# Optimization experiments

Measured on AMD Instinct MI355X. Metric: run time of the kernel, lower is better.

The kernel has to match this reference:

```python
import jax, jax.numpy as jnp
import numpy as np

B, N, E = 4, 20000, 320000
DA, DB, H, OUT = 64, 64, 128, 1  # feature dims, hidden_dim, output_dim; DA+DB == H


def setup_inputs() -> dict:
    key = jax.random.key(0)
    ks = jax.random.split(key, 9)
    feat_a = jax.random.normal(ks[0], (B, N, DA), dtype=jnp.float32)
    feat_b = jax.random.normal(ks[1], (B, N, DB), dtype=jnp.float32)
    edge_index = jax.random.randint(ks[2], (2, E), 0, N)
    s = 1.0 / np.sqrt(H)
    W_gcn = jax.random.normal(ks[3], (H, H), dtype=jnp.float32) * s
    b_gcn = jnp.zeros((H,), dtype=jnp.float32)
    W1 = jax.random.normal(ks[4], (H, H), dtype=jnp.float32) * s
    b1 = jax.random.normal(ks[5], (H,), dtype=jnp.float32) * 0.01
    W2 = jax.random.normal(ks[6], (H, OUT), dtype=jnp.float32) * s
    b2 = jnp.zeros((OUT,), dtype=jnp.float32)
    return {"feat_a": feat_a, "feat_b": feat_b, "edge_index": edge_index,
            "W_gcn": W_gcn, "b_gcn": b_gcn, "W1": W1, "b1": b1, "W2": W2, "b2": b2}


def _gcn_conv(x, src, dst, W, b):
    # x: [B, N, H_in]; GCNConv: out = D^-1/2 (A+I) D^-1/2 (x W) + b
    n = x.shape[1]
    loops = jnp.arange(n)
    src_sl = jnp.concatenate([src, loops])  # add self-loops
    dst_sl = jnp.concatenate([dst, loops])
    deg = jax.ops.segment_sum(jnp.ones_like(src_sl, dtype=x.dtype), dst_sl, num_segments=n)
    dinv = jnp.where(deg > 0, jax.lax.rsqrt(deg), 0.0)
    norm = dinv[src_sl] * dinv[dst_sl]  # [E+N]
    h = x @ W  # [B, N, H]

    def agg(hb):  # hb: [N, H]
        msgs = hb[src_sl] * norm[:, None]  # gather + scale, [E+N, H]
        return jax.ops.segment_sum(msgs, dst_sl, num_segments=n)  # scatter-add

    return jax.vmap(agg)(h) + b


def reference(feat_a, feat_b, edge_index, W_gcn, b_gcn, W1, b1, W2, b2):
    combined = jnp.concatenate([feat_a, feat_b], axis=-1)  # [B, N, H]
    gcn_out = _gcn_conv(combined, edge_index[0], edge_index[1], W_gcn, b_gcn)
    pooled = gcn_out.mean(axis=1)  # mean over nodes -> [B, H]
    hid = jax.nn.relu(pooled @ W1 + b1)  # dropout is identity in eval
    logits = hid @ W2 + b2  # [B, 1]
    return logits
```

## Files before the change

### kernel.cpp

```cpp
#include <hip/hip_runtime.h>

#define NB 4
#define NN 20000
#define NE 320000
#define HH 128

#define EBLK 64
#define HTHR 1024
#define CHUNKS 128
#define WTHR 512
#define PER ((NN + CHUNKS - 1) / CHUNKS)
#define TOTW (CHUNKS * NB)

#define OFF_PDEG 0
#define OFF_DINV (EBLK * NN)
#define OFF_PS   (OFF_DINV + NN)
#define OFF_V    (OFF_PS + EBLK * NN)
#define OFF_CNT  (OFF_V + NB * HH)

__global__ void __launch_bounds__(HTHR) deg_hist_kernel(
        const int* __restrict__ dst, float* __restrict__ pdeg) {
    __shared__ float hist[NN];
    const int t = threadIdx.x, bk = blockIdx.x;
    for (int i = t; i < NN; i += HTHR) hist[i] = 0.0f;
    __syncthreads();
    for (int e = bk * HTHR + t; e < NE; e += EBLK * HTHR)
        atomicAdd(&hist[dst[e]], 1.0f);
    __syncthreads();
    float* out = pdeg + (size_t)bk * NN;
    for (int i = t; i < NN; i += HTHR) out[i] = hist[i];
}

__global__ void reduce_deg_kernel(const float* __restrict__ pdeg,
                                  float* __restrict__ dinv,
                                  float* __restrict__ v, int* __restrict__ counter) {
    if (blockIdx.x == 0) {
        v[threadIdx.x] = 0.0f;
        v[threadIdx.x + 256] = 0.0f;
        if (threadIdx.x == 0) *counter = 0;
    }
    const int n = blockIdx.x * 256 + threadIdx.x;
    if (n >= NN) return;
    float acc = 1.0f;
    #pragma unroll 8
    for (int c = 0; c < EBLK; ++c) acc += pdeg[(size_t)c * NN + n];
    dinv[n] = rsqrtf(acc);
}

__global__ void __launch_bounds__(HTHR) s_hist_kernel(
        const int* __restrict__ src, const int* __restrict__ dst,
        const float* __restrict__ dinv, float* __restrict__ ps) {
    __shared__ float hist[NN];
    const int t = threadIdx.x, bk = blockIdx.x;
    for (int i = t; i < NN; i += HTHR) hist[i] = 0.0f;
    __syncthreads();
    for (int e = bk * HTHR + t; e < NE; e += EBLK * HTHR)
        atomicAdd(&hist[src[e]], dinv[dst[e]]);
    __syncthreads();
    float* out = ps + (size_t)bk * NN;
    for (int i = t; i < NN; i += HTHR) out[i] = hist[i];
}

__global__ void __launch_bounds__(WTHR) wsum_mlp_kernel(
        const float* __restrict__ fa, const float* __restrict__ fb,
        const float* __restrict__ dinv, const float* __restrict__ ps,
        const float* __restrict__ Wg, const float* __restrict__ bg,
        const float* __restrict__ W1, const float* __restrict__ b1,
        const float* __restrict__ W2, const float* __restrict__ b2,
        float* __restrict__ v, int* __restrict__ counter,
        float* __restrict__ out) {
    __shared__ float wl[PER];
    __shared__ float4 smem[WTHR];
    __shared__ int lastflag;
    const int t = threadIdx.x;
    const int c = blockIdx.x, b = blockIdx.y;
    const int n0 = c * PER;
    const int n1 = min(NN, n0 + PER);
    const int cnt = n1 - n0;

    for (int i = t; i < cnt; i += WTHR) {
        const int n = n0 + i;
        float acc = 0.0f;
        #pragma unroll 8
        for (int cc = 0; cc < EBLK; ++cc) acc += ps[(size_t)cc * NN + n];
        const float di = dinv[n];
        wl[i] = di * (di + acc);
    }
    __syncthreads();

    const int g = t >> 5;
    const int q = t & 31;
    const float* base = (q < 16)
        ? (fa + (size_t)b * NN * 64 + (size_t)q * 4)
        : (fb + (size_t)b * NN * 64 + (size_t)(q - 16) * 4);

    float4 acc = make_float4(0.f, 0.f, 0.f, 0.f);
    for (int n = n0 + g; n < n1; n += 16) {
        float wn = wl[n - n0];
        float4 x = *reinterpret_cast<const float4*>(base + (size_t)n * 64);
        acc.x += wn * x.x; acc.y += wn * x.y; acc.z += wn * x.z; acc.w += wn * x.w;
    }

    smem[t] = acc;
    __syncthreads();
    if (t < 32) {
        float4 r = smem[t];
        #pragma unroll
        for (int gg = 1; gg < 16; ++gg) {
            float4 o = smem[gg * 32 + t];
            r.x += o.x; r.y += o.y; r.z += o.z; r.w += o.w;
        }
        const int k = (t < 16) ? t * 4 : 64 + (t - 16) * 4;
        float* vb = v + b * HH + k;
        atomicAdd(vb + 0, r.x);
        atomicAdd(vb + 1, r.y);
        atomicAdd(vb + 2, r.z);
        atomicAdd(vb + 3, r.w);
    }
    if (t == 0) {
        asm volatile("s_waitcnt vmcnt(0)" ::: "memory");
        int old = atomicAdd(counter, 1);
        lastflag = (old == TOTW - 1);
    }
    __syncthreads();
    if (!lastflag) return;

    __shared__ float xs[NB][HH];
    __shared__ float ys[NB][HH];
    __shared__ float red[NB][HH];
    const int bb = t >> 7;
    const int kk = t & (HH - 1);

    float val = atomicAdd(&v[t], 0.0f);
    xs[bb][kk] = val * (1.0f / NN);
    __syncthreads();

    float a1 = bg[kk];
    #pragma unroll 8
    for (int j = 0; j < HH; ++j) a1 += xs[bb][j] * Wg[j * HH + kk];
    ys[bb][kk] = a1;
    __syncthreads();

    float a2 = b1[kk];
    #pragma unroll 8
    for (int j = 0; j < HH; ++j) a2 += ys[bb][j] * W1[j * HH + kk];
    a2 = fmaxf(a2, 0.0f);
    red[bb][kk] = a2 * W2[kk];
    __syncthreads();

    #pragma unroll
    for (int off = HH / 2; off > 0; off >>= 1) {
        if (kk < off) red[bb][kk] += red[bb][kk + off];
        __syncthreads();
    }
    if (kk == 0) out[bb] = red[bb][0] + b2[0];
}

extern "C" void kernel_launch(void* const* d_in, const int* in_sizes, int n_in,
                              void* d_out, int out_size, void* d_ws, size_t ws_size,
                              hipStream_t stream) {
    const float* fa = (const float*)d_in[0];
    const float* fb = (const float*)d_in[1];
    const int*   ei = (const int*)d_in[2];
    const float* Wg = (const float*)d_in[3];
    const float* bg = (const float*)d_in[4];
    const float* W1 = (const float*)d_in[5];
    const float* b1 = (const float*)d_in[6];
    const float* W2 = (const float*)d_in[7];
    const float* b2 = (const float*)d_in[8];
    float* out = (float*)d_out;

    const int* src = ei;
    const int* dst = ei + NE;

    float* ws   = (float*)d_ws;
    float* pdeg = ws + OFF_PDEG;
    float* dinv = ws + OFF_DINV;
    float* ps   = ws + OFF_PS;
    float* v    = ws + OFF_V;
    int* counter = (int*)(ws + OFF_CNT);

    deg_hist_kernel<<<EBLK, HTHR, 0, stream>>>(dst, pdeg);

    const int rb = (NN + 255) / 256;
    reduce_deg_kernel<<<rb, 256, 0, stream>>>(pdeg, dinv, v, counter);

    s_hist_kernel<<<EBLK, HTHR, 0, stream>>>(src, dst, dinv, ps);

    dim3 grid(CHUNKS, NB);
    wsum_mlp_kernel<<<grid, WTHR, 0, stream>>>(fa, fb, dinv, ps,
                                               Wg, bg, W1, b1, W2, b2,
                                               v, counter, out);
}
```

Before: 62.92 us.

## Process all batches per node chunk and split ps reduction across threads

The weighted-sum kernel now launches one block per node chunk, with 256 chunks, and loops over all four batches inside. This removes the fourfold recomputation of per-node weights from the 64 partial histograms that the old per-batch grid did. The ps column reduction is split eight ways across threads to add parallelism. Extra blocks in reduce_deg prefetch the MLP weights into cache, and the final matvec loops are unrolled further. In exchange, each block serialises four reduction and atomic rounds, and the grid has fewer blocks (256 instead of 512).

```diff
diff --git a/kernel.cpp b/kernel.cpp
--- a/kernel.cpp
+++ b/kernel.cpp
@@ -7,10 +7,13 @@
 
 #define EBLK 64
 #define HTHR 1024
-#define CHUNKS 128
+#define CHUNKS 256
 #define WTHR 512
-#define PER ((NN + CHUNKS - 1) / CHUNKS)
-#define TOTW (CHUNKS * NB)
+#define PER 79
+#define TOTW CHUNKS
+
+#define RB 79
+#define WARMB 17
 
 #define OFF_PDEG 0
 #define OFF_DINV (EBLK * NN)
@@ -33,7 +36,29 @@
 
 __global__ void reduce_deg_kernel(const float* __restrict__ pdeg,
                                   float* __restrict__ dinv,
-                                  float* __restrict__ v, int* __restrict__ counter) {
+                                  float* __restrict__ v, int* __restrict__ counter,
+                                  const float* __restrict__ Wg,
+                                  const float* __restrict__ W1,
+                                  const float* __restrict__ bg,
+                                  const float* __restrict__ b1,
+                                  const float* __restrict__ W2) {
+    if (blockIdx.x >= RB) {
+        const int wt = (blockIdx.x - RB) * 256 + threadIdx.x;
+        float a = 0.0f;
+        if (wt < HH * HH / 4) {
+            float4 x = ((const float4*)Wg)[wt];
+            float4 y = ((const float4*)W1)[wt];
+            a = x.x + x.w + y.x + y.w;
+        } else if (wt < HH * HH / 4 + HH / 4) {
+            const int i = wt - HH * HH / 4;
+            float4 x = ((const float4*)bg)[i];
+            float4 y = ((const float4*)b1)[i];
+            float4 z = ((const float4*)W2)[i];
+            a = x.x + y.x + z.x;
+        }
+        asm volatile("" :: "v"(a));
+        return;
+    }
     if (blockIdx.x == 0) {
         v[threadIdx.x] = 0.0f;
         v[threadIdx.x + 256] = 0.0f;
@@ -70,53 +95,76 @@
         float* __restrict__ v, int* __restrict__ counter,
         float* __restrict__ out) {
     __shared__ float wl[PER];
+    __shared__ float wpart[PER][8];
     __shared__ float4 smem[WTHR];
     __shared__ int lastflag;
     const int t = threadIdx.x;
-    const int c = blockIdx.x, b = blockIdx.y;
+    const int c = blockIdx.x;
     const int n0 = c * PER;
     const int n1 = min(NN, n0 + PER);
     const int cnt = n1 - n0;
 
-    for (int i = t; i < cnt; i += WTHR) {
-        const int n = n0 + i;
-        float acc = 0.0f;
-        #pragma unroll 8
-        for (int cc = 0; cc < EBLK; ++cc) acc += ps[(size_t)cc * NN + n];
-        const float di = dinv[n];
-        wl[i] = di * (di + acc);
-    }
-    __syncthreads();
-
-    const int g = t >> 5;
-    const int q = t & 31;
-    const float* base = (q < 16)
-        ? (fa + (size_t)b * NN * 64 + (size_t)q * 4)
-        : (fb + (size_t)b * NN * 64 + (size_t)(q - 16) * 4);
-
-    float4 acc = make_float4(0.f, 0.f, 0.f, 0.f);
-    for (int n = n0 + g; n < n1; n += 16) {
-        float wn = wl[n - n0];
-        float4 x = *reinterpret_cast<const float4*>(base + (size_t)n * 64);
-        acc.x += wn * x.x; acc.y += wn * x.y; acc.z += wn * x.z; acc.w += wn * x.w;
-    }
-
-    smem[t] = acc;
-    __syncthreads();
-    if (t < 32) {
-        float4 r = smem[t];
+    if (cnt > 0) {
+        for (int idx = t; idx < cnt * 8; idx += WTHR) {
+            const int i = idx >> 3, s = idx & 7;
+            const int n = n0 + i;
+            float a = 0.0f;
+            #pragma unroll
+            for (int u = 0; u < 8; ++u) a += ps[(size_t)(s * 8 + u) * NN + n];
+            wpart[i][s] = a;
+        }
+        __syncthreads();
+        for (int i = t; i < cnt; i += WTHR) {
+            float a = 0.0f;
+            #pragma unroll
+            for (int s = 0; s < 8; ++s) a += wpart[i][s];
+            const float di = dinv[n0 + i];
+            wl[i] = di * (di + a);
+        }
+        __syncthreads();
+
+        const int g = t >> 5;
+        const int q = t & 31;
+        const float* base = (q < 16) ? (fa + (size_t)q * 4)
+                                     : (fb + (size_t)(q - 16) * 4);
+
+        float4 acc[NB];
         #pragma unroll
-        for (int gg = 1; gg < 16; ++gg) {
-            float4 o = smem[gg * 32 + t];
-            r.x += o.x; r.y += o.y; r.z += o.z; r.w += o.w;
-        }
-        const int k = (t < 16) ? t * 4 : 64 + (t - 16) * 4;
-        float* vb = v + b * HH + k;
-        atomicAdd(vb + 0, r.x);
-        atomicAdd(vb + 1, r.y);
-        atomicAdd(vb + 2, r.z);
-        atomicAdd(vb + 3, r.w);
-    }
+        for (int b = 0; b < NB; ++b) acc[b] = make_float4(0.f, 0.f, 0.f, 0.f);
+
+        for (int n = n0 + g; n < n1; n += 16) {
+            const float wn = wl[n - n0];
+            #pragma unroll
+            for (int b = 0; b < NB; ++b) {
+                float4 x = *reinterpret_cast<const float4*>(
+                    base + ((size_t)b * NN + n) * 64);
+                acc[b].x += wn * x.x; acc[b].y += wn * x.y;
+                acc[b].z += wn * x.z; acc[b].w += wn * x.w;
+            }
+        }
+
+        #pragma unroll
+        for (int b = 0; b < NB; ++b) {
+            smem[t] = acc[b];
+            __syncthreads();
+            if (t < 32) {
+                float4 r = smem[t];
+                #pragma unroll
+                for (int gg = 1; gg < 16; ++gg) {
+                    float4 o = smem[gg * 32 + t];
+                    r.x += o.x; r.y += o.y; r.z += o.z; r.w += o.w;
+                }
+                const int k = (t < 16) ? t * 4 : 64 + (t - 16) * 4;
+                float* vb = v + b * HH + k;
+                atomicAdd(vb + 0, r.x);
+                atomicAdd(vb + 1, r.y);
+                atomicAdd(vb + 2, r.z);
+                atomicAdd(vb + 3, r.w);
+            }
+            __syncthreads();
+        }
+    }
+
     if (t == 0) {
         asm volatile("s_waitcnt vmcnt(0)" ::: "memory");
         int old = atomicAdd(counter, 1);
@@ -136,13 +184,13 @@
     __syncthreads();
 
     float a1 = bg[kk];
-    #pragma unroll 8
+    #pragma unroll 16
     for (int j = 0; j < HH; ++j) a1 += xs[bb][j] * Wg[j * HH + kk];
     ys[bb][kk] = a1;
     __syncthreads();
 
     float a2 = b1[kk];
-    #pragma unroll 8
+    #pragma unroll 16
     for (int j = 0; j < HH; ++j) a2 += ys[bb][j] * W1[j * HH + kk];
     a2 = fmaxf(a2, 0.0f);
     red[bb][kk] = a2 * W2[kk];
@@ -182,13 +230,12 @@
 
     deg_hist_kernel<<<EBLK, HTHR, 0, stream>>>(dst, pdeg);
 
-    const int rb = (NN + 255) / 256;
-    reduce_deg_kernel<<<rb, 256, 0, stream>>>(pdeg, dinv, v, counter);
+    reduce_deg_kernel<<<RB + WARMB, 256, 0, stream>>>(pdeg, dinv, v, counter,
+                                                      Wg, W1, bg, b1, W2);
 
     s_hist_kernel<<<EBLK, HTHR, 0, stream>>>(src, dst, dinv, ps);
 
-    dim3 grid(CHUNKS, NB);
-    wsum_mlp_kernel<<<grid, WTHR, 0, stream>>>(fa, fb, dinv, ps,
-                                               Wg, bg, W1, b1, W2, b2,
-                                               v, counter, out);
-}
+    wsum_mlp_kernel<<<CHUNKS, WTHR, 0, stream>>>(fa, fb, dinv, ps,
+                                                 Wg, bg, W1, b1, W2, b2,
+                                                 v, counter, out);
+}
```

Measured after the change: 71.31 us. +13.3%, slower.

## Fuse source-weight histogram and weighted feature sum into one cooperative kernel

Applied to the files above, without the earlier changes.

The separate s_hist and wsum_mlp kernels become a single 256-block cooperative kernel. Each block builds an LDS histogram over its edge slice and folds it into a global per-node array with sparse atomics. A two-level counter barrier then gates the weighted feature reduction, where each block covers 80 nodes for all four batches with 8-way split output accumulators. The last block prefetches the weights and runs the MLP once every block finishes. This removes a kernel launch and the 64-way partial-histogram rereads, at the cost of spin-wait barriers and more contended global atomics.

```diff
diff --git a/kernel.cpp b/kernel.cpp
--- a/kernel.cpp
+++ b/kernel.cpp
@@ -7,21 +7,31 @@
 
 #define EBLK 64
 #define HTHR 1024
-#define CHUNKS 128
-#define WTHR 512
-#define PER ((NN + CHUNKS - 1) / CHUNKS)
-#define TOTW (CHUNKS * NB)
+#define RB 79
+
+#define FBLK 256
+#define FTHR 1024
+#define SEDG (NE / FBLK)
+#define WBLK 250
+#define PER 80
+#define NSEC 8
 
 #define OFF_PDEG 0
 #define OFF_DINV (EBLK * NN)
-#define OFF_PS   (OFF_DINV + NN)
-#define OFF_V    (OFF_PS + EBLK * NN)
-#define OFF_CNT  (OFF_V + NB * HH)
+#define OFF_S    (OFF_DINV + NN)
+#define OFF_V    (OFF_S + NN)
+#define OFF_CNT  (OFF_V + NSEC * NB * HH)
 
 __global__ void __launch_bounds__(HTHR) deg_hist_kernel(
-        const int* __restrict__ dst, float* __restrict__ pdeg) {
+        const int* __restrict__ dst, float* __restrict__ pdeg,
+        float* __restrict__ s, float* __restrict__ v, int* __restrict__ cnts) {
     __shared__ float hist[NN];
     const int t = threadIdx.x, bk = blockIdx.x;
+    if (bk == 0) {
+        for (int i = t; i < NN; i += HTHR) s[i] = 0.0f;
+        for (int i = t; i < NSEC * NB * HH; i += HTHR) v[i] = 0.0f;
+        if (t < 18) cnts[t] = 0;
+    }
     for (int i = t; i < NN; i += HTHR) hist[i] = 0.0f;
     __syncthreads();
     for (int e = bk * HTHR + t; e < NE; e += EBLK * HTHR)
@@ -32,13 +42,7 @@
 }
 
 __global__ void reduce_deg_kernel(const float* __restrict__ pdeg,
-                                  float* __restrict__ dinv,
-                                  float* __restrict__ v, int* __restrict__ counter) {
-    if (blockIdx.x == 0) {
-        v[threadIdx.x] = 0.0f;
-        v[threadIdx.x + 256] = 0.0f;
-        if (threadIdx.x == 0) *counter = 0;
-    }
+                                  float* __restrict__ dinv) {
     const int n = blockIdx.x * 256 + threadIdx.x;
     if (n >= NN) return;
     float acc = 1.0f;
@@ -47,113 +51,160 @@
     dinv[n] = rsqrtf(acc);
 }
 
-__global__ void __launch_bounds__(HTHR) s_hist_kernel(
-        const int* __restrict__ src, const int* __restrict__ dst,
-        const float* __restrict__ dinv, float* __restrict__ ps) {
-    __shared__ float hist[NN];
+#define FMA4(D, W, X) { D.x += (W)*(X).x; D.y += (W)*(X).y; \
+                        D.z += (W)*(X).z; D.w += (W)*(X).w; }
+
+__global__ void __launch_bounds__(FTHR) fused_kernel(
+    const float* __restrict__ fa, const float* __restrict__ fb,
+    const int* __restrict__ src, const int* __restrict__ dst,
+    const float* __restrict__ dinv, float* __restrict__ s,
+    const float* __restrict__ Wg, const float* __restrict__ bg,
+    const float* __restrict__ W1, const float* __restrict__ b1,
+    const float* __restrict__ W2, const float* __restrict__ b2,
+    float* __restrict__ v, int* __restrict__ cnts, float* __restrict__ out)
+{
+    __shared__ __align__(16) float sh[NN];
+    int* subS = cnts;
+    int* masS = cnts + 8;
+    int* subW = cnts + 9;
+    int* masW = cnts + 17;
     const int t = threadIdx.x, bk = blockIdx.x;
-    for (int i = t; i < NN; i += HTHR) hist[i] = 0.0f;
-    __syncthreads();
-    for (int e = bk * HTHR + t; e < NE; e += EBLK * HTHR)
-        atomicAdd(&hist[src[e]], dinv[dst[e]]);
-    __syncthreads();
-    float* out = ps + (size_t)bk * NN;
-    for (int i = t; i < NN; i += HTHR) out[i] = hist[i];
-}
-
-__global__ void __launch_bounds__(WTHR) wsum_mlp_kernel(
-        const float* __restrict__ fa, const float* __restrict__ fb,
-        const float* __restrict__ dinv, const float* __restrict__ ps,
-        const float* __restrict__ Wg, const float* __restrict__ bg,
-        const float* __restrict__ W1, const float* __restrict__ b1,
-        const float* __restrict__ W2, const float* __restrict__ b2,
-        float* __restrict__ v, int* __restrict__ counter,
-        float* __restrict__ out) {
-    __shared__ float wl[PER];
-    __shared__ float4 smem[WTHR];
-    __shared__ int lastflag;
-    const int t = threadIdx.x;
-    const int c = blockIdx.x, b = blockIdx.y;
-    const int n0 = c * PER;
-    const int n1 = min(NN, n0 + PER);
-    const int cnt = n1 - n0;
-
-    for (int i = t; i < cnt; i += WTHR) {
-        const int n = n0 + i;
-        float acc = 0.0f;
-        #pragma unroll 8
-        for (int cc = 0; cc < EBLK; ++cc) acc += ps[(size_t)cc * NN + n];
-        const float di = dinv[n];
-        wl[i] = di * (di + acc);
-    }
-    __syncthreads();
-
-    const int g = t >> 5;
-    const int q = t & 31;
-    const float* base = (q < 16)
-        ? (fa + (size_t)b * NN * 64 + (size_t)q * 4)
-        : (fb + (size_t)b * NN * 64 + (size_t)(q - 16) * 4);
-
-    float4 acc = make_float4(0.f, 0.f, 0.f, 0.f);
-    for (int n = n0 + g; n < n1; n += 16) {
-        float wn = wl[n - n0];
-        float4 x = *reinterpret_cast<const float4*>(base + (size_t)n * 64);
-        acc.x += wn * x.x; acc.y += wn * x.y; acc.z += wn * x.z; acc.w += wn * x.w;
-    }
-
-    smem[t] = acc;
-    __syncthreads();
-    if (t < 32) {
-        float4 r = smem[t];
-        #pragma unroll
-        for (int gg = 1; gg < 16; ++gg) {
-            float4 o = smem[gg * 32 + t];
-            r.x += o.x; r.y += o.y; r.z += o.z; r.w += o.w;
-        }
-        const int k = (t < 16) ? t * 4 : 64 + (t - 16) * 4;
-        float* vb = v + b * HH + k;
-        atomicAdd(vb + 0, r.x);
-        atomicAdd(vb + 1, r.y);
-        atomicAdd(vb + 2, r.z);
-        atomicAdd(vb + 3, r.w);
-    }
+
+    for (int i = t; i < NN; i += FTHR) sh[i] = 0.0f;
+    __syncthreads();
+    {
+        const int e0 = bk * SEDG;
+        for (int e = e0 + t; e < e0 + SEDG; e += FTHR)
+            atomicAdd(&sh[src[e]], dinv[dst[e]]);
+    }
+    __syncthreads();
+    for (int i = t; i < NN; i += FTHR) {
+        const float hv = sh[i];
+        if (hv != 0.0f) atomicAdd(&s[i], hv);
+    }
+    __syncthreads();
+    if (t == 0) {
+        int old = atomicAdd(&subS[bk & 7], 1);
+        if (old == FBLK / NSEC - 1) atomicAdd(masS, 1);
+    }
+
+    if (bk < WBLK) {
+        if (t == 0) {
+            while (atomicAdd(masS, 0) < NSEC) __builtin_amdgcn_s_sleep(16);
+        }
+        __syncthreads();
+
+        const int n0 = bk * PER;
+        if (t < PER) {
+            const int n = n0 + t;
+            const float sv = atomicAdd(&s[n], 0.0f);
+            const float di = dinv[n];
+            sh[t] = di * (di + sv);
+        }
+        __syncthreads();
+
+        const int g = t >> 5, q = t & 31;
+        const float wA = sh[g], wB = sh[g + 32];
+        const bool three = (t < 512);
+        const float wC = three ? sh[g + 64] : 0.0f;
+        __syncthreads();
+
+        const float* base = (q < 16) ? (fa + (size_t)q * 4)
+                                     : (fb + (size_t)(q - 16) * 4);
+        const int nA = n0 + g, nB = n0 + g + 32, nC = n0 + g + 64;
+        #define LD(B, N) (*reinterpret_cast<const float4*>( \
+                              base + ((size_t)(B) * NN + (N)) * 64))
+        float4 xA0 = LD(0, nA), xA1 = LD(1, nA), xA2 = LD(2, nA), xA3 = LD(3, nA);
+        float4 xB0 = LD(0, nB), xB1 = LD(1, nB), xB2 = LD(2, nB), xB3 = LD(3, nB);
+        float4 ac0 = make_float4(0.f, 0.f, 0.f, 0.f);
+        float4 ac1 = ac0, ac2 = ac0, ac3 = ac0;
+        FMA4(ac0, wA, xA0) FMA4(ac1, wA, xA1) FMA4(ac2, wA, xA2) FMA4(ac3, wA, xA3)
+        FMA4(ac0, wB, xB0) FMA4(ac1, wB, xB1) FMA4(ac2, wB, xB2) FMA4(ac3, wB, xB3)
+        if (three) {
+            float4 xC0 = LD(0, nC), xC1 = LD(1, nC), xC2 = LD(2, nC), xC3 = LD(3, nC);
+            FMA4(ac0, wC, xC0) FMA4(ac1, wC, xC1) FMA4(ac2, wC, xC2) FMA4(ac3, wC, xC3)
+        }
+
+        float4* sm = reinterpret_cast<float4*>(sh);
+        float* vsec = v + (size_t)(bk & (NSEC - 1)) * (NB * HH);
+        #define PHASE(AC, B) { \
+            sm[t] = AC; __syncthreads(); \
+            if (t < 32) { \
+                float4 r = sm[t]; \
+                _Pragma("unroll") \
+                for (int gg = 1; gg < 32; ++gg) { \
+                    float4 o = sm[gg * 32 + t]; \
+                    r.x += o.x; r.y += o.y; r.z += o.z; r.w += o.w; } \
+                const int k = (t < 16) ? t * 4 : 64 + (t - 16) * 4; \
+                float* vb = vsec + (B) * HH + k; \
+                atomicAdd(vb + 0, r.x); atomicAdd(vb + 1, r.y); \
+                atomicAdd(vb + 2, r.z); atomicAdd(vb + 3, r.w); } \
+            __syncthreads(); }
+        PHASE(ac0, 0) PHASE(ac1, 1) PHASE(ac2, 2) PHASE(ac3, 3)
+    }
+
     if (t == 0) {
         asm volatile("s_waitcnt vmcnt(0)" ::: "memory");
-        int old = atomicAdd(counter, 1);
-        lastflag = (old == TOTW - 1);
-    }
-    __syncthreads();
-    if (!lastflag) return;
-
-    __shared__ float xs[NB][HH];
-    __shared__ float ys[NB][HH];
-    __shared__ float red[NB][HH];
-    const int bb = t >> 7;
-    const int kk = t & (HH - 1);
-
-    float val = atomicAdd(&v[t], 0.0f);
-    xs[bb][kk] = val * (1.0f / NN);
-    __syncthreads();
-
-    float a1 = bg[kk];
-    #pragma unroll 8
-    for (int j = 0; j < HH; ++j) a1 += xs[bb][j] * Wg[j * HH + kk];
-    ys[bb][kk] = a1;
-    __syncthreads();
-
-    float a2 = b1[kk];
-    #pragma unroll 8
-    for (int j = 0; j < HH; ++j) a2 += ys[bb][j] * W1[j * HH + kk];
-    a2 = fmaxf(a2, 0.0f);
-    red[bb][kk] = a2 * W2[kk];
-    __syncthreads();
-
-    #pragma unroll
-    for (int off = HH / 2; off > 0; off >>= 1) {
-        if (kk < off) red[bb][kk] += red[bb][kk + off];
-        __syncthreads();
-    }
-    if (kk == 0) out[bb] = red[bb][0] + b2[0];
+        int old = atomicAdd(&subW[bk & 7], 1);
+        if (old == FBLK / NSEC - 1) atomicAdd(masW, 1);
+    }
+
+    if (bk == FBLK - 1) {
+        float warm = 0.0f;
+        for (int i = t; i < HH * HH / 4; i += FTHR) {
+            float4 a = ((const float4*)Wg)[i];
+            float4 b = ((const float4*)W1)[i];
+            warm += a.x + a.w + b.x + b.w;
+        }
+        asm volatile("" :: "v"(warm));
+        if (t == 0) {
+            while (atomicAdd(masW, 0) < NSEC) __builtin_amdgcn_s_sleep(16);
+        }
+        __syncthreads();
+
+        float* xs  = sh;
+        float* ys  = sh + 512;
+        float* red = sh + 1024;
+        const int half = t >> 9;
+        const int idx  = t & 511;
+        const int bb = idx >> 7, kk = idx & 127;
+
+        if (t < 512) {
+            float val = 0.0f;
+            #pragma unroll
+            for (int sct = 0; sct < NSEC; ++sct)
+                val += atomicAdd(&v[sct * (NB * HH) + t], 0.0f);
+            xs[t] = val * (1.0f / NN);
+        }
+        __syncthreads();
+
+        float p1 = (half == 0) ? bg[kk] : 0.0f;
+        #pragma unroll 8
+        for (int j = half * 64; j < half * 64 + 64; ++j)
+            p1 += xs[bb * HH + j] * Wg[j * HH + kk];
+        if (half == 1) red[idx] = p1;
+        __syncthreads();
+        if (half == 0) ys[idx] = p1 + red[idx];
+        __syncthreads();
+
+        float p2 = (half == 0) ? b1[kk] : 0.0f;
+        #pragma unroll 8
+        for (int j = half * 64; j < half * 64 + 64; ++j)
+            p2 += ys[bb * HH + j] * W1[j * HH + kk];
+        if (half == 1) red[idx] = p2;
+        __syncthreads();
+        if (half == 0) {
+            float h = fmaxf(p2 + red[idx], 0.0f);
+            red[idx] = h * W2[kk];
+        }
+        __syncthreads();
+
+        for (int off = 64; off > 0; off >>= 1) {
+            if (t < 512 && kk < off) red[bb * HH + kk] += red[bb * HH + kk + off];
+            __syncthreads();
+        }
+        if (t < 512 && kk == 0) out[bb] = red[bb * HH] + b2[0];
+    }
 }
 
 extern "C" void kernel_launch(void* const* d_in, const int* in_sizes, int n_in,
@@ -176,19 +227,26 @@
     float* ws   = (float*)d_ws;
     float* pdeg = ws + OFF_PDEG;
     float* dinv = ws + OFF_DINV;
-    float* ps   = ws + OFF_PS;
+    float* s    = ws + OFF_S;
     float* v    = ws + OFF_V;
-    int* counter = (int*)(ws + OFF_CNT);
-
-    deg_hist_kernel<<<EBLK, HTHR, 0, stream>>>(dst, pdeg);
-
-    const int rb = (NN + 255) / 256;
-    reduce_deg_kernel<<<rb, 256, 0, stream>>>(pdeg, dinv, v, counter);
-
-    s_hist_kernel<<<EBLK, HTHR, 0, stream>>>(src, dst, dinv, ps);
-
-    dim3 grid(CHUNKS, NB);
-    wsum_mlp_kernel<<<grid, WTHR, 0, stream>>>(fa, fb, dinv, ps,
-                                               Wg, bg, W1, b1, W2, b2,
-                                               v, counter, out);
-}
+    int*   cnts = (int*)(ws + OFF_CNT);
+
+    deg_hist_kernel<<<EBLK, HTHR, 0, stream>>>(dst, pdeg, s, v, cnts);
+
+    reduce_deg_kernel<<<RB, 256, 0, stream>>>(pdeg, dinv);
+
+    void* args[] = {
+        (void*)&fa, (void*)&fb, (void*)&src, (void*)&dst,
+        (void*)&dinv, (void*)&s,
+        (void*)&Wg, (void*)&bg, (void*)&W1, (void*)&b1,
+        (void*)&W2, (void*)&b2,
+        (void*)&v, (void*)&cnts, (void*)&out
+    };
+    hipError_t cerr = hipLaunchCooperativeKernel((void*)fused_kernel,
+                                                 dim3(FBLK), dim3(FTHR),
+                                                 args, 0, stream);
+    if (cerr != hipSuccess) {
+        fused_kernel<<<dim3(FBLK), dim3(FTHR), 0, stream>>>(
+            fa, fb, src, dst, dinv, s, Wg, bg, W1, b1, W2, b2, v, cnts, out);
+    }
+}
```

After: 84.88 us. +34.9%, slower.
